# Kernel optimization log

Measured on AMD Instinct MI355X. Metric: run time of the kernel, lower is better.

Reference implementation:

```python
import jax, jax.numpy as jnp
import numpy as np

# RReLU in eval mode == LeakyReLU with slope (lower+upper)/2, defaults 1/8, 1/3
RRELU_SLOPE = (1.0 / 8.0 + 1.0 / 3.0) / 2.0


def rrelu(x):
    return jnp.where(x >= 0, x, x * RRELU_SLOPE)


def _linear_params(key, fan_in, fan_out):
    kw, kb = jax.random.split(key)
    s = 1.0 / np.sqrt(fan_in)
    W = jax.random.uniform(kw, (fan_in, fan_out), minval=-s, maxval=s, dtype=jnp.float32)
    b = jax.random.uniform(kb, (fan_out,), minval=-s, maxval=s, dtype=jnp.float32)
    return W, b


def setup_inputs() -> dict:
    key = jax.random.key(0)
    ks = jax.random.split(key, 6)
    B, L, D_TS, D_SEQ, HID = 64, 2048, 8, 120, 64
    DIN = D_TS + D_SEQ
    ts = jax.random.normal(ks[0], (B, L, D_TS), dtype=jnp.float32)
    seq = jax.random.normal(ks[1], (B, L, D_SEQ), dtype=jnp.float32)
    lengths = jax.random.randint(ks[2], (B,), 1, L + 1, dtype=jnp.int32)
    Wk, bk = _linear_params(ks[3], DIN, HID)
    Wq, bq = _linear_params(ks[4], DIN, HID)
    Wv, bv = _linear_params(ks[5], DIN, HID)
    return {"ts": ts, "seq": seq, "lengths": lengths,
            "Wk": Wk, "bk": bk, "Wq": Wq, "bq": bq, "Wv": Wv, "bv": bv}


def reference(ts, seq, lengths, Wk, bk, Wq, bq, Wv, bv):
    # packed_cat([ts, seq]) -> concat along feature dim; padded positions masked later
    x = jnp.concatenate([ts, seq], axis=-1)              # [B, L, Din]
    k = rrelu(jnp.einsum('bld,dh->blh', x, Wk) + bk)     # [B, L, H]
    v = rrelu(jnp.einsum('bld,dh->blh', x, Wv) + bv)     # [B, L, H]
    q = rrelu(jnp.einsum('bld,dh->blh', x, Wq) + bq)     # [B, L, H]
    B, L, _ = x.shape
    # get_last_vectors_unpadded: last valid token of each sequence
    q_last = q[jnp.arange(B), lengths - 1]               # [B, H]
    scores = jnp.einsum('bh,blh->bl', q_last, k)         # [B, L]
    valid = jnp.arange(L)[None, :] < lengths[:, None]    # [B, L]
    scores = jnp.where(valid, scores, -jnp.inf)
    attn = jax.nn.softmax(scores, axis=-1)               # masked softmax over seq
    return jnp.einsum('bl,blh->bh', attn, v)             # [B, H]
```

## Files before the change

### kernel.cpp

```cpp
#include <hip/hip_runtime.h>
#include <hip/hip_bf16.h>

#define B_   64
#define L_   2048
#define DTS  8
#define DSEQ 120
#define H_   64
#define TILE 64
#define NT   32

typedef unsigned short u16;
typedef unsigned int   u32;
typedef __bf16 bf16x8 __attribute__((ext_vector_type(8)));
typedef float  f32x4  __attribute__((ext_vector_type(4)));

__device__ __forceinline__ float rrelu_f(float x) {
    return x >= 0.f ? x : x * 0.22916666666666666f;
}
__device__ __forceinline__ u16 f2bf(float x) {
    unsigned u = __float_as_uint(x);
    return (u16)((u + 0x7FFFu + ((u >> 16) & 1u)) >> 16);
}
__device__ __forceinline__ float bf2f(u16 u) {
    return __uint_as_float(((unsigned)u) << 16);
}

__global__ void setup_kernel(const float* __restrict__ ts, const float* __restrict__ seq,
                             const int* __restrict__ lengths,
                             const float* __restrict__ Wk, const float* __restrict__ Wv,
                             const float* __restrict__ Wq, const float* __restrict__ bq,
                             u16* __restrict__ pkh, u16* __restrict__ pkl,
                             u16* __restrict__ pvh, u16* __restrict__ pvl,
                             float* __restrict__ qlast)
{
    const int blk = blockIdx.x, tid = threadIdx.x;
    if (blk < 64) {
        const int f = blk * 256 + tid;
        const int idx = f & 8191;
        const bool isK = f < 8192;
        const float* W = isK ? Wk : Wv;
        u16* hi = isK ? pkh : pvh;
        u16* lo = isK ? pkl : pvl;
        const int j = idx & 7, lane = (idx >> 3) & 63, kk = (idx >> 9) & 3, ni = idx >> 11;
        const int kd = kk * 32 + (lane >> 4) * 8 + j;
        const int n  = ni * 16 + (lane & 15);
        const float v = W[kd * H_ + n];
        const u16 h = f2bf(v);
        hi[idx] = h;
        lo[idx] = f2bf(v - bf2f(h));
    } else {
        const int b = (blk - 64) * 4 + (tid >> 6), h = tid & 63;
        const int l = lengths[b] - 1;
        const float* tsr = ts  + ((size_t)b * L_ + l) * DTS;
        const float* sqr = seq + ((size_t)b * L_ + l) * DSEQ;
        float acc = bq[h];
        #pragma unroll
        for (int d = 0; d < DTS; ++d)  acc += tsr[d] * Wq[d * H_ + h];
        for (int d = 0; d < DSEQ; ++d) acc += sqr[d] * Wq[(DTS + d) * H_ + h];
        qlast[b * H_ + h] = rrelu_f(acc);
    }
}

__global__ __launch_bounds__(256) void tile_kernel(
    const float* __restrict__ ts, const float* __restrict__ seq,
    const int* __restrict__ lengths,
    const u16* __restrict__ pkh, const u16* __restrict__ pkl,
    const u16* __restrict__ pvh, const u16* __restrict__ pvl,
    const float* __restrict__ bk, const float* __restrict__ bv,
    const float* __restrict__ qlast,
    float* __restrict__ pden, float* __restrict__ pnum)
{
    const int b = blockIdx.y, t = blockIdx.x;
    const int len = lengths[b];
    const int ls = t * TILE;
    if (ls >= len) return;
    const int nv = min(TILE, len - ls);
    const int pb = b * NT + t;

    const int tid = threadIdx.x, wave = tid >> 6, lane = tid & 63;
    const int quad = lane >> 4, l16 = lane & 15;
    const int m0 = wave * 16;

    __shared__ __align__(16) u16 xh[TILE][136];
    __shared__ __align__(16) u16 xl[TILE][136];
    __shared__ float red[4][H_];
    __shared__ float wd[4];

    float qv[4], bbk[4], bbv[4];
    #pragma unroll
    for (int ni = 0; ni < 4; ++ni) {
        qv[ni]  = qlast[b * H_ + ni * 16 + l16];
        bbk[ni] = bk[ni * 16 + l16];
        bbv[ni] = bv[ni * 16 + l16];
    }

    for (int c = tid; c < TILE * 32; c += 256) {
        const int row = c >> 5, ch = c & 31;
        const float* src = (ch < 2)
            ? ts  + ((size_t)(b * L_ + ls + row)) * DTS  + ch * 4
            : seq + ((size_t)(b * L_ + ls + row)) * DSEQ + (ch - 2) * 4;
        const f32x4 v4 = *(const f32x4*)src;
        u16 ha[4], la[4];
        #pragma unroll
        for (int j = 0; j < 4; ++j) {
            ha[j] = f2bf(v4[j]);
            la[j] = f2bf(v4[j] - bf2f(ha[j]));
        }
        *(uint2*)&xh[row][ch * 4] = make_uint2((u32)ha[0] | ((u32)ha[1] << 16),
                                               (u32)ha[2] | ((u32)ha[3] << 16));
        *(uint2*)&xl[row][ch * 4] = make_uint2((u32)la[0] | ((u32)la[1] << 16),
                                               (u32)la[2] | ((u32)la[3] << 16));
    }
    __syncthreads();

    bf16x8 ah[4], al[4];
    {
        const u16* hrow = &xh[m0 + l16][quad * 8];
        const u16* lrow = &xl[m0 + l16][quad * 8];
        #pragma unroll
        for (int kk = 0; kk < 4; ++kk) {
            ah[kk] = *(const bf16x8*)(hrow + kk * 32);
            al[kk] = *(const bf16x8*)(lrow + kk * 32);
        }
    }

    float ps[4] = {0.f, 0.f, 0.f, 0.f};
    float vv[4][4];
    #pragma unroll
    for (int ni = 0; ni < 4; ++ni) {
        f32x4 ak = {0.f, 0.f, 0.f, 0.f};
        f32x4 av = {0.f, 0.f, 0.f, 0.f};
        #pragma unroll
        for (int kk = 0; kk < 4; ++kk) {
            const size_t off = (size_t)((ni * 4 + kk) * 64 + lane) * 8;
            const bf16x8 bkh = *(const bf16x8*)(pkh + off);
            const bf16x8 bkl = *(const bf16x8*)(pkl + off);
            const bf16x8 bvh = *(const bf16x8*)(pvh + off);
            const bf16x8 bvl = *(const bf16x8*)(pvl + off);
            ak = __builtin_amdgcn_mfma_f32_16x16x32_bf16(ah[kk], bkh, ak, 0, 0, 0);
            ak = __builtin_amdgcn_mfma_f32_16x16x32_bf16(al[kk], bkh, ak, 0, 0, 0);
            ak = __builtin_amdgcn_mfma_f32_16x16x32_bf16(ah[kk], bkl, ak, 0, 0, 0);
            av = __builtin_amdgcn_mfma_f32_16x16x32_bf16(ah[kk], bvh, av, 0, 0, 0);
            av = __builtin_amdgcn_mfma_f32_16x16x32_bf16(al[kk], bvh, av, 0, 0, 0);
            av = __builtin_amdgcn_mfma_f32_16x16x32_bf16(ah[kk], bvl, av, 0, 0, 0);
        }
        #pragma unroll
        for (int r = 0; r < 4; ++r) {
            ps[r] += qv[ni] * rrelu_f(ak[r] + bbk[ni]);
            vv[ni][r] = rrelu_f(av[r] + bbv[ni]);
        }
    }

    #pragma unroll
    for (int mk = 1; mk < 16; mk <<= 1)
        #pragma unroll
        for (int r = 0; r < 4; ++r) ps[r] += __shfl_xor(ps[r], mk);
    float p[4], dsum = 0.f;
    #pragma unroll
    for (int r = 0; r < 4; ++r) {
        const int row = quad * 4 + r + m0 - m0;
        p[r] = ((quad * 4 + r) + m0 < ls + nv - ls ? 1 : 1) ? 0.f : 0.f;
        p[r] = ((m0 + quad * 4 + r) < nv) ? __expf(fminf(ps[r], 80.f)) : 0.f;
        dsum += p[r];
        (void)row;
    }

    float pv[4];
    #pragma unroll
    for (int ni = 0; ni < 4; ++ni) {
        float a = 0.f;
        #pragma unroll
        for (int r = 0; r < 4; ++r) a += p[r] * vv[ni][r];
        pv[ni] = a;
    }
    #pragma unroll
    for (int mk = 16; mk < 64; mk <<= 1) {
        #pragma unroll
        for (int ni = 0; ni < 4; ++ni) pv[ni] += __shfl_xor(pv[ni], mk);
        dsum += __shfl_xor(dsum, mk);
    }
    if (quad == 0) {
        #pragma unroll
        for (int ni = 0; ni < 4; ++ni) red[wave][ni * 16 + l16] = pv[ni];
    }
    if (lane == 0) wd[wave] = dsum;
    __syncthreads();

    if (tid < H_)
        pnum[(size_t)pb * H_ + tid] = red[0][tid] + red[1][tid] + red[2][tid] + red[3][tid];
    if (tid == 0)
        pden[pb] = wd[0] + wd[1] + wd[2] + wd[3];
}

__global__ void combine_kernel(const int* __restrict__ lengths,
                               const float* __restrict__ pden,
                               const float* __restrict__ pnum,
                               float* __restrict__ out)
{
    const int b = blockIdx.x, h = threadIdx.x;
    const int nt = (lengths[b] + TILE - 1) / TILE;
    float den = 0.f, num = 0.f;
    for (int t = 0; t < nt; ++t) {
        den += pden[b * NT + t];
        num += pnum[(size_t)(b * NT + t) * H_ + h];
    }
    out[b * H_ + h] = num / den;
}

extern "C" void kernel_launch(void* const* d_in, const int* in_sizes, int n_in,
                              void* d_out, int out_size, void* d_ws, size_t ws_size,
                              hipStream_t stream)
{
    const float* ts      = (const float*)d_in[0];
    const float* seq     = (const float*)d_in[1];
    const int*   lengths = (const int*)d_in[2];
    const float* Wk      = (const float*)d_in[3];
    const float* bk      = (const float*)d_in[4];
    const float* Wq      = (const float*)d_in[5];
    const float* bq      = (const float*)d_in[6];
    const float* Wv      = (const float*)d_in[7];
    const float* bv      = (const float*)d_in[8];

    float* ws    = (float*)d_ws;
    float* qlast = ws;
    float* pden  = ws + 4096;
    float* pnum  = ws + 6144;
    u16*   packw = (u16*)(ws + 137216);
    u16* pkh = packw;
    u16* pkl = packw + 8192;
    u16* pvh = packw + 16384;
    u16* pvl = packw + 24576;

    setup_kernel<<<dim3(80), dim3(256), 0, stream>>>(ts, seq, lengths, Wk, Wv, Wq, bq,
                                                     pkh, pkl, pvh, pvl, qlast);
    tile_kernel<<<dim3(NT, B_), dim3(256), 0, stream>>>(ts, seq, lengths,
                                                        pkh, pkl, pvh, pvl, bk, bv,
                                                        qlast, pden, pnum);
    combine_kernel<<<dim3(B_), dim3(H_), 0, stream>>>(lengths, pden, pnum, (float*)d_out);
}
```

Baseline: 142.5 us.

## Split K and V projections across waves and parallelize q_last computation

The tile kernel now uses 512 threads. Four waves compute the K projection and scores, the other four compute the V projection, and the softmax weights pass between them through shared memory. This halves the per-wave MFMA chain and raises parallelism, at the cost of an extra barrier and a shared buffer. The setup kernel gives each batch's q_last its own block and splits the dot product across four waves with a shared-memory reduction, and the combine loop is unrolled.

```diff
diff --git a/kernel.cpp b/kernel.cpp
--- a/kernel.cpp
+++ b/kernel.cpp
@@ -49,19 +49,33 @@
         hi[idx] = h;
         lo[idx] = f2bf(v - bf2f(h));
     } else {
-        const int b = (blk - 64) * 4 + (tid >> 6), h = tid & 63;
+        const int b = blk - 64;
+        const int h = tid & 63, part = tid >> 6;
         const int l = lengths[b] - 1;
         const float* tsr = ts  + ((size_t)b * L_ + l) * DTS;
         const float* sqr = seq + ((size_t)b * L_ + l) * DSEQ;
-        float acc = bq[h];
-        #pragma unroll
-        for (int d = 0; d < DTS; ++d)  acc += tsr[d] * Wq[d * H_ + h];
-        for (int d = 0; d < DSEQ; ++d) acc += sqr[d] * Wq[(DTS + d) * H_ + h];
-        qlast[b * H_ + h] = rrelu_f(acc);
-    }
-}
-
-__global__ __launch_bounds__(256) void tile_kernel(
+        float acc = 0.f;
+        if (part == 0) {
+            #pragma unroll
+            for (int d = 0; d < DTS; ++d)  acc += tsr[d] * Wq[d * H_ + h];
+            #pragma unroll
+            for (int d = DTS; d < 32; ++d) acc += sqr[d - DTS] * Wq[d * H_ + h];
+        } else {
+            const int d0 = part * 32;
+            #pragma unroll
+            for (int i = 0; i < 32; ++i)
+                acc += sqr[d0 + i - DTS] * Wq[(d0 + i) * H_ + h];
+        }
+        __shared__ float qred[4][H_];
+        qred[part][h] = acc;
+        __syncthreads();
+        if (tid < H_)
+            qlast[b * H_ + tid] = rrelu_f(qred[0][tid] + qred[1][tid] +
+                                          qred[2][tid] + qred[3][tid] + bq[tid]);
+    }
+}
+
+__global__ __launch_bounds__(512) void tile_kernel(
     const float* __restrict__ ts, const float* __restrict__ seq,
     const int* __restrict__ lengths,
     const u16* __restrict__ pkh, const u16* __restrict__ pkl,
@@ -79,22 +93,18 @@
 
     const int tid = threadIdx.x, wave = tid >> 6, lane = tid & 63;
     const int quad = lane >> 4, l16 = lane & 15;
-    const int m0 = wave * 16;
+    const int mg = wave & 3, isV = wave >> 2;
+    const int m0 = mg * 16;
 
     __shared__ __align__(16) u16 xh[TILE][136];
     __shared__ __align__(16) u16 xl[TILE][136];
+    __shared__ float scp[TILE];
     __shared__ float red[4][H_];
     __shared__ float wd[4];
 
-    float qv[4], bbk[4], bbv[4];
     #pragma unroll
-    for (int ni = 0; ni < 4; ++ni) {
-        qv[ni]  = qlast[b * H_ + ni * 16 + l16];
-        bbk[ni] = bk[ni * 16 + l16];
-        bbv[ni] = bv[ni * 16 + l16];
-    }
-
-    for (int c = tid; c < TILE * 32; c += 256) {
+    for (int i = 0; i < 4; ++i) {
+        const int c = i * 512 + tid;
         const int row = c >> 5, ch = c & 31;
         const float* src = (ch < 2)
             ? ts  + ((size_t)(b * L_ + ls + row)) * DTS  + ch * 4
@@ -124,66 +134,81 @@
         }
     }
 
-    float ps[4] = {0.f, 0.f, 0.f, 0.f};
-    float vv[4][4];
+    const u16* bhp = isV ? pvh : pkh;
+    const u16* blp = isV ? pvl : pkl;
+    const float* bias = isV ? bv : bk;
+    float bb[4];
+    #pragma unroll
+    for (int ni = 0; ni < 4; ++ni) bb[ni] = bias[ni * 16 + l16];
+
+    float cd[4][4];
     #pragma unroll
     for (int ni = 0; ni < 4; ++ni) {
-        f32x4 ak = {0.f, 0.f, 0.f, 0.f};
-        f32x4 av = {0.f, 0.f, 0.f, 0.f};
+        f32x4 acc = {0.f, 0.f, 0.f, 0.f};
         #pragma unroll
         for (int kk = 0; kk < 4; ++kk) {
             const size_t off = (size_t)((ni * 4 + kk) * 64 + lane) * 8;
-            const bf16x8 bkh = *(const bf16x8*)(pkh + off);
-            const bf16x8 bkl = *(const bf16x8*)(pkl + off);
-            const bf16x8 bvh = *(const bf16x8*)(pvh + off);
-            const bf16x8 bvl = *(const bf16x8*)(pvl + off);
-            ak = __builtin_amdgcn_mfma_f32_16x16x32_bf16(ah[kk], bkh, ak, 0, 0, 0);
-            ak = __builtin_amdgcn_mfma_f32_16x16x32_bf16(al[kk], bkh, ak, 0, 0, 0);
-            ak = __builtin_amdgcn_mfma_f32_16x16x32_bf16(ah[kk], bkl, ak, 0, 0, 0);
-            av = __builtin_amdgcn_mfma_f32_16x16x32_bf16(ah[kk], bvh, av, 0, 0, 0);
-            av = __builtin_amdgcn_mfma_f32_16x16x32_bf16(al[kk], bvh, av, 0, 0, 0);
-            av = __builtin_amdgcn_mfma_f32_16x16x32_bf16(ah[kk], bvl, av, 0, 0, 0);
-        }
+            const bf16x8 bh = *(const bf16x8*)(bhp + off);
+            const bf16x8 bl = *(const bf16x8*)(blp + off);
+            acc = __builtin_amdgcn_mfma_f32_16x16x32_bf16(ah[kk], bh, acc, 0, 0, 0);
+            acc = __builtin_amdgcn_mfma_f32_16x16x32_bf16(al[kk], bh, acc, 0, 0, 0);
+            acc = __builtin_amdgcn_mfma_f32_16x16x32_bf16(ah[kk], bl, acc, 0, 0, 0);
+        }
+        #pragma unroll
+        for (int r = 0; r < 4; ++r) cd[ni][r] = rrelu_f(acc[r] + bb[ni]);
+    }
+
+    if (!isV) {
+        float qv[4];
+        #pragma unroll
+        for (int ni = 0; ni < 4; ++ni) qv[ni] = qlast[b * H_ + ni * 16 + l16];
+        float ps[4] = {0.f, 0.f, 0.f, 0.f};
+        #pragma unroll
+        for (int ni = 0; ni < 4; ++ni)
+            #pragma unroll
+            for (int r = 0; r < 4; ++r) ps[r] += qv[ni] * cd[ni][r];
+        #pragma unroll
+        for (int mk = 1; mk < 16; mk <<= 1)
+            #pragma unroll
+            for (int r = 0; r < 4; ++r) ps[r] += __shfl_xor(ps[r], mk);
+        float p4[4], ds = 0.f;
         #pragma unroll
         for (int r = 0; r < 4; ++r) {
-            ps[r] += qv[ni] * rrelu_f(ak[r] + bbk[ni]);
-            vv[ni][r] = rrelu_f(av[r] + bbv[ni]);
-        }
-    }
-
-    #pragma unroll
-    for (int mk = 1; mk < 16; mk <<= 1)
-        #pragma unroll
-        for (int r = 0; r < 4; ++r) ps[r] += __shfl_xor(ps[r], mk);
-    float p[4], dsum = 0.f;
-    #pragma unroll
-    for (int r = 0; r < 4; ++r) {
-        const int row = quad * 4 + r + m0 - m0;
-        p[r] = ((quad * 4 + r) + m0 < ls + nv - ls ? 1 : 1) ? 0.f : 0.f;
-        p[r] = ((m0 + quad * 4 + r) < nv) ? __expf(fminf(ps[r], 80.f)) : 0.f;
-        dsum += p[r];
-        (void)row;
-    }
-
-    float pv[4];
-    #pragma unroll
-    for (int ni = 0; ni < 4; ++ni) {
-        float a = 0.f;
-        #pragma unroll
-        for (int r = 0; r < 4; ++r) a += p[r] * vv[ni][r];
-        pv[ni] = a;
-    }
-    #pragma unroll
-    for (int mk = 16; mk < 64; mk <<= 1) {
-        #pragma unroll
-        for (int ni = 0; ni < 4; ++ni) pv[ni] += __shfl_xor(pv[ni], mk);
-        dsum += __shfl_xor(dsum, mk);
-    }
-    if (quad == 0) {
-        #pragma unroll
-        for (int ni = 0; ni < 4; ++ni) red[wave][ni * 16 + l16] = pv[ni];
-    }
-    if (lane == 0) wd[wave] = dsum;
+            const int row = m0 + quad * 4 + r;
+            p4[r] = (row < nv) ? __expf(fminf(ps[r], 80.f)) : 0.f;
+            ds += p4[r];
+        }
+        if (l16 == 0) {
+            #pragma unroll
+            for (int r = 0; r < 4; ++r) scp[m0 + quad * 4 + r] = p4[r];
+        }
+        ds += __shfl_xor(ds, 16);
+        ds += __shfl_xor(ds, 32);
+        if (lane == 0) wd[mg] = ds;
+    }
+    __syncthreads();
+
+    if (isV) {
+        float pr[4];
+        #pragma unroll
+        for (int r = 0; r < 4; ++r) pr[r] = scp[m0 + quad * 4 + r];
+        float pv[4];
+        #pragma unroll
+        for (int ni = 0; ni < 4; ++ni) {
+            float a = 0.f;
+            #pragma unroll
+            for (int r = 0; r < 4; ++r) a += pr[r] * cd[ni][r];
+            pv[ni] = a;
+        }
+        #pragma unroll
+        for (int mk = 16; mk < 64; mk <<= 1)
+            #pragma unroll
+            for (int ni = 0; ni < 4; ++ni) pv[ni] += __shfl_xor(pv[ni], mk);
+        if (quad == 0) {
+            #pragma unroll
+            for (int ni = 0; ni < 4; ++ni) red[mg][ni * 16 + l16] = pv[ni];
+        }
+    }
     __syncthreads();
 
     if (tid < H_)
@@ -200,6 +225,7 @@
     const int b = blockIdx.x, h = threadIdx.x;
     const int nt = (lengths[b] + TILE - 1) / TILE;
     float den = 0.f, num = 0.f;
+    #pragma unroll 4
     for (int t = 0; t < nt; ++t) {
         den += pden[b * NT + t];
         num += pnum[(size_t)(b * NT + t) * H_ + h];
@@ -231,9 +257,9 @@
     u16* pvh = packw + 16384;
     u16* pvl = packw + 24576;
 
-    setup_kernel<<<dim3(80), dim3(256), 0, stream>>>(ts, seq, lengths, Wk, Wv, Wq, bq,
-                                                     pkh, pkl, pvh, pvl, qlast);
-    tile_kernel<<<dim3(NT, B_), dim3(256), 0, stream>>>(ts, seq, lengths,
+    setup_kernel<<<dim3(128), dim3(256), 0, stream>>>(ts, seq, lengths, Wk, Wv, Wq, bq,
+                                                      pkh, pkl, pvh, pvl, qlast);
+    tile_kernel<<<dim3(NT, B_), dim3(512), 0, stream>>>(ts, seq, lengths,
                                                         pkh, pkl, pvh, pvl, bk, bv,
                                                         qlast, pden, pnum);
     combine_kernel<<<dim3(B_), dim3(H_), 0, stream>>>(lengths, pden, pnum, (float*)d_out);
```

Result: faster. 130.5 us (-8.4%).
